# Kernel tuning notes

Measured on AMD Instinct MI355X. Metric: run time of the kernel, lower is better.

The kernel has to match this reference:

```python
import jax, jax.numpy as jnp
import numpy as np

DILATIONS = (1, 3, 6, 12)          # layer dilations, flattened from [[1,3],[6,12]]
BLOCKS = ((0, 1), (2, 3))           # block -> layer indices
H_SIZE = 32
STATE_SIZE = 128
OUT_SIZE = STATE_SIZE - H_SIZE      # 96
INPUT_SIZE = 64
OUTPUT_SIZE = 64
T, B = 512, 512


def _linear_params(k, fan_in, fan_out):
    bound = 1.0 / np.sqrt(fan_in)
    kw, kb = jax.random.split(k)
    W = jax.random.uniform(kw, (fan_out, fan_in), minval=-bound, maxval=bound, dtype=jnp.float32)
    b = jax.random.uniform(kb, (fan_out,), minval=-bound, maxval=bound, dtype=jnp.float32)
    return W, b


def setup_inputs() -> dict:
    key = jax.random.key(0)
    ks = jax.random.split(key, 8)
    x = jax.random.normal(ks[0], (T, B, INPUT_SIZE), dtype=jnp.float32)
    ins = [INPUT_SIZE, OUT_SIZE, OUT_SIZE, OUT_SIZE]  # first layer sees raw input
    out = {"x": x}
    for l in range(4):
        W, b = _linear_params(ks[1 + l], ins[l] + 2 * H_SIZE, 4 * STATE_SIZE)
        out[f"W{l}"] = W
        out[f"b{l}"] = b
    Wa, ba = _linear_params(ks[5], OUT_SIZE, OUTPUT_SIZE)
    out["Wa"] = Wa
    out["ba"] = ba
    return out


def _s2cell(W, b, inp, prev_h, second_h, prev_c, delayed_c, has_prev, has_del):
    # xh = cat(input, prev_h, delayed_h-or-prev_h) ; zeros when no prev state (handled by caller masks)
    xh = jnp.concatenate([inp, prev_h, second_h], axis=1)
    g = xh @ W.T + b                                     # [B, 4*state]
    g0, g1, g2, g3 = jnp.split(g, 4, axis=1)
    forget = jax.nn.sigmoid(g0 + 1.0)
    cand = jnp.tanh(g1)
    alpha = jax.nn.sigmoid(g2)
    out_gate = jax.nn.sigmoid(g3)
    weighted = jnp.where(has_del, alpha * prev_c + (1.0 - alpha) * delayed_c, prev_c)
    new_c = jnp.where(has_prev, forget * weighted + (1.0 - forget) * cand, cand)
    whole = out_gate * new_c
    return whole[:, :OUT_SIZE], whole[:, OUT_SIZE:], new_c


def reference(x, W0, b0, W1, b1, W2, b2, W3, b3, Wa, ba):
    Ws = [W0, W1, W2, W3]
    bs = [b0, b1, b2, b3]
    batch = x.shape[1]
    h0 = tuple(jnp.zeros((d, batch, H_SIZE), jnp.float32) for d in DILATIONS)
    c0 = tuple(jnp.zeros((d, batch, STATE_SIZE), jnp.float32) for d in DILATIONS)

    def step(carry, inp_t):
        t, h_bufs, c_bufs = carry
        h_bufs = list(h_bufs)
        c_bufs = list(c_bufs)
        has_prev = t >= 1
        prev_block = None
        out_t = None
        for iblock, layers in enumerate(BLOCKS):
            for j, l in enumerate(layers):
                cur_in = (inp_t if iblock == 0 else prev_block) if j == 0 else out_t
                d = DILATIONS[l]
                # ring buffer: slot (t-1)%d holds state at t-1, slot t%d still holds state at t-d
                prev_h = jnp.where(has_prev, h_bufs[l][(t - 1) % d], 0.0)
                prev_c = c_bufs[l][(t - 1) % d]
                has_del = t >= d
                del_h = jnp.where(has_del, h_bufs[l][t % d], prev_h)
                del_c = c_bufs[l][t % d]
                out_t, new_h, new_c = _s2cell(Ws[l], bs[l], cur_in, prev_h, del_h,
                                              prev_c, del_c, has_prev, has_del)
                h_bufs[l] = h_bufs[l].at[t % d].set(new_h)
                c_bufs[l] = c_bufs[l].at[t % d].set(new_c)
            prev_block = out_t if iblock == 0 else out_t + prev_block  # resnet shortcut
        y = prev_block @ Wa.T + ba
        return (t + 1, tuple(h_bufs), tuple(c_bufs)), y

    _, ys = jax.lax.scan(step, (jnp.int32(0), h0, c0), x)
    return ys  # [T, B, output_size]
```

## Files before the change

### kernel.cpp

```cpp
#include <hip/hip_runtime.h>

typedef unsigned int uint;
typedef unsigned short ushort;
typedef unsigned long long u64;
typedef __attribute__((ext_vector_type(8))) short bf16x8;
typedef __attribute__((ext_vector_type(4))) float f32x4;

#define T_STEPS 512
#define BATCH   512
#define NB      8
#define RD      16
#define XS      168
#define CSTR    12
#define OUTC    96
#define FSTR    32

__device__ __forceinline__ ushort f2bf(float f){
  uint u = __builtin_bit_cast(uint, f);
  u = (u + 0x7FFFu + ((u >> 16) & 1u)) >> 16;
  return (ushort)u;
}
__device__ __forceinline__ float bf2f(ushort h){
  uint u = ((uint)h) << 16; return __builtin_bit_cast(float, u);
}
__device__ __forceinline__ float sigm(float x){
  float e = __builtin_exp2f(-1.44269504f * x);
  return __builtin_amdgcn_rcpf(1.0f + e);
}
__device__ __forceinline__ float tanh_fast(float x){
  float e = __builtin_exp2f(-2.88539008f * x);
  return 2.0f * __builtin_amdgcn_rcpf(1.0f + e) - 1.0f;
}
__device__ __forceinline__ uint aload32(const uint* p){
  return __hip_atomic_load(p, __ATOMIC_RELAXED, __HIP_MEMORY_SCOPE_AGENT);
}
__device__ __forceinline__ void astore32(uint* p, uint v){
  __hip_atomic_store(p, v, __ATOMIC_RELAXED, __HIP_MEMORY_SCOPE_AGENT);
}
__device__ __forceinline__ u64 aload64(const u64* p){
  return __hip_atomic_load(p, __ATOMIC_RELAXED, __HIP_MEMORY_SCOPE_AGENT);
}
__device__ __forceinline__ void astore64(u64* p, u64 v){
  __hip_atomic_store(p, v, __ATOMIC_RELAXED, __HIP_MEMORY_SCOPE_AGENT);
}

__global__ __launch_bounds__(512, 1)
void rnn_pipeline(const float* __restrict__ x,
                  const float* __restrict__ W0, const float* __restrict__ b0,
                  const float* __restrict__ W1, const float* __restrict__ b1,
                  const float* __restrict__ W2, const float* __restrict__ b2,
                  const float* __restrict__ W3, const float* __restrict__ b3,
                  const float* __restrict__ Wa, const float* __restrict__ ba,
                  float* __restrict__ y_out,
                  uint* __restrict__ prod, uint* __restrict__ consA,
                  uint* __restrict__ consB,
                  u64* __restrict__ hop0, u64* __restrict__ hop1,
                  u64* __restrict__ hop2)
{
  const int tid  = threadIdx.x;
  const int wv   = tid >> 6;
  const int lane = tid & 63;
  const int l15  = lane & 15;
  const int hi   = lane >> 4;
  const int rep  = blockIdx.x & 63;
  const int stage= blockIdx.x >> 6;
  const int b0r  = rep * NB;

  const int dil = (stage==0)?1:(stage==1)?3:(stage==2)?6:12;
  const int KIN = (stage==0)?64:96;
  const int K   = KIN + 64;
  const float* Wl = (stage==0)?W0:(stage==1)?W1:(stage==2)?W2:W3;
  const float* bl = (stage==0)?b0:(stage==1)?b1:(stage==2)?b2:b3;

  __shared__ __align__(16) ushort xh_hi[16*XS], xh_lo[16*XS];
  __shared__ __align__(16) float  sh_c[12*128*CSTR];
  __shared__ __align__(16) ushort h_hi[12*NB*32], h_lo[12*NB*32];
  __shared__ __align__(16) ushort outp[2304];
  __shared__ __align__(16) ushort o1p[1536];
  __shared__ __align__(16) float  o3f[NB*OUTC];
  __shared__ __align__(16) float  yst[512];

  for (int i = tid; i < 16*XS; i += 512){ xh_hi[i] = 0; xh_lo[i] = 0; }
  for (int i = tid; i < 12*128*CSTR; i += 512) sh_c[i] = 0.0f;
  for (int i = tid; i < 12*NB*32; i += 512){ h_hi[i] = 0; h_lo[i] = 0; }
  for (int i = tid; i < 2304; i += 512) outp[i] = 0;
  for (int i = tid; i < 1536; i += 512) o1p[i] = 0;
  for (int i = tid; i < NB*OUTC; i += 512) o3f[i] = 0.0f;

  const int sidx = 16*wv + l15;

  bf16x8 whi[4][5], wlo[4][5];
  #pragma unroll
  for (int j = 0; j < 4; ++j){
    const int grow = 128*j + sidx;
    #pragma unroll
    for (int ks = 0; ks < 5; ++ks){
      bf16x8 vh, vl;
      const int cb = ks*32 + hi*8;
      if (cb < K){
        const float* p = Wl + (size_t)grow*K + cb;
        #pragma unroll
        for (int i = 0; i < 8; ++i){
          float w = p[i];
          ushort h = f2bf(w);
          vh[i] = (short)h;
          vl[i] = (short)f2bf(w - bf2f(h));
        }
      } else {
        #pragma unroll
        for (int i = 0; i < 8; ++i){ vh[i] = 0; vl[i] = 0; }
      }
      whi[j][ks] = vh; wlo[j][ks] = vl;
    }
  }
  float bias[4];
  #pragma unroll
  for (int j = 0; j < 4; ++j) bias[j] = bl[128*j + sidx];

  bf16x8 phi[3], plo[3];
  #pragma unroll
  for (int ks = 0; ks < 3; ++ks){
    bf16x8 z;
    #pragma unroll
    for (int i = 0; i < 8; ++i) z[i]=0;
    phi[ks]=z; plo[ks]=z;
  }
  float bav = 0.0f;
  if (stage == 3 && wv < 4){
    const int ocol = 16*wv + l15;
    #pragma unroll
    for (int ks = 0; ks < 3; ++ks){
      const float* p = Wa + (size_t)ocol*96 + ks*32 + hi*8;
      bf16x8 vh, vl;
      #pragma unroll
      for (int i = 0; i < 8; ++i){
        float w = p[i];
        ushort h = f2bf(w);
        vh[i] = (short)h;
        vl[i] = (short)f2bf(w - bf2f(h));
      }
      phi[ks] = vh; plo[ks] = vl;
    }
    bav = ba[ocol];
  }

  uint* up_prod  = (stage==1)? &prod[rep*FSTR] : (stage==2)? &prod[(64+rep)*FSTR] :
                   (stage==3)? &prod[(128+rep)*FSTR] : nullptr;
  uint* up_prod1 = (stage==3)? &prod[(64+rep)*FSTR] : nullptr;
  uint* my_prod  = (stage==0)? &prod[rep*FSTR] : (stage==1)? &prod[(64+rep)*FSTR] :
                   (stage==2)? &prod[(128+rep)*FSTR] : nullptr;
  uint* my_consA = (stage==1)? &consA[rep*FSTR] : (stage==2)? &consA[(64+rep)*FSTR] :
                   (stage==3)? &consA[(128+rep)*FSTR] : nullptr;
  uint* my_consB = (stage==3)? &consB[rep*FSTR] : nullptr;
  uint* dnA      = (stage==0)? &consA[rep*FSTR] : (stage==1)? &consA[(64+rep)*FSTR] :
                   (stage==2)? &consA[(128+rep)*FSTR] : nullptr;
  uint* dnB      = (stage==1)? &consB[rep*FSTR] : nullptr;
  const u64* hop_in  = (stage==1)? hop0 : (stage==2)? hop1 : nullptr;
  u64*       hop_out = (stage==0)? hop0 : (stage==1)? hop1 : (stage==2)? hop2 : nullptr;

  __syncthreads();

  u64 pfA = 0, pfB = 0; float xv = 0.0f;
  uint fvU = 0, fvU1 = 0, fvDA = 0, fvDB = 0;
  if (stage == 0){
    xv = x[(size_t)(b0r + (tid>>6))*64 + (tid&63)];
  } else if (stage < 3){
    do { fvU = aload32(up_prod); if (fvU < 3u) __builtin_amdgcn_s_sleep(2); } while (fvU < 3u);
    if (tid < 384) pfA = aload64(hop_in + (size_t)rep*384 + tid);
  } else {
    do { fvU  = aload32(up_prod);  if (fvU  < 3u) __builtin_amdgcn_s_sleep(2); } while (fvU  < 3u);
    do { fvU1 = aload32(up_prod1); if (fvU1 < 3u) __builtin_amdgcn_s_sleep(2); } while (fvU1 < 3u);
    const u64* s2 = hop2 + (size_t)rep*384;
    const u64* s1 = hop1 + (size_t)rep*384;
    pfA = (tid < 384) ? aload64(s2 + tid) : aload64(s1 + (tid - 384));
    if (tid < 256) pfB = aload64(s1 + 128 + tid);
  }

  int cur = 0, prv = dil - 1;
  for (int t = 0; t < T_STEPS; ++t){
    const int slot = t & (RD-1);

    if (stage < 3) asm volatile("s_waitcnt vmcnt(1)" ::: "memory");
    if (stage > 0){
      const bool bad = (fvU < (uint)(t+3)) || (stage==3 && fvU1 < (uint)(t+3));
      if (bad){
        if (lane == 0){
          while (aload32(up_prod) < (uint)(t+1)) __builtin_amdgcn_s_sleep(2);
          if (stage == 3)
            while (aload32(up_prod1) < (uint)(t+1)) __builtin_amdgcn_s_sleep(2);
        }
        if (stage < 3){
          if (tid < 384) pfA = aload64(hop_in + (size_t)(slot*64 + rep)*384 + tid);
        } else {
          const u64* s2 = hop2 + (size_t)(slot*64 + rep)*384;
          const u64* s1 = hop1 + (size_t)(slot*64 + rep)*384;
          pfA = (tid < 384) ? aload64(s2 + tid) : aload64(s1 + (tid - 384));
          if (tid < 256) pfB = aload64(s1 + 128 + tid);
        }
      }
    }
    if (stage == 0){
      const int r = tid >> 6, c = tid & 63;
      ushort hb = f2bf(xv);
      xh_hi[r*XS + c] = hb;
      xh_lo[r*XS + c] = f2bf(xv - bf2f(hb));
    } else {
      if (tid < 384){
        const int q = (tid < 192) ? tid : tid - 192;
        ushort* plane = (tid < 192) ? xh_hi : xh_lo;
        const int r = q / 24, c4 = (q % 24) * 4;
        *(u64*)(plane + r*XS + c4) = pfA;
      } else if (stage == 3){
        *(u64*)(o1p + 4*(tid - 384)) = pfA;
      }
      if (stage == 3 && tid < 256) *(u64*)(o1p + 4*(128 + tid)) = pfB;
    }
    {
      const int which = tid >> 8, rem = tid & 255, r = rem >> 5, c = rem & 31;
      const int srcslot = (which == 1 && t >= dil) ? cur : prv;
      xh_hi[r*XS + KIN + which*32 + c] = h_hi[srcslot*(NB*32) + r*32 + c];
      xh_lo[r*XS + KIN + which*32 + c] = h_lo[srcslot*(NB*32) + r*32 + c];
    }
    __syncthreads();
    if (tid == 0){
      if (stage > 0){
        astore32(my_consA, (uint)(t+1));
        if (stage == 3) astore32(my_consB, (uint)(t+1));
      }
      if (stage < 3 && t >= 1) astore32(my_prod, (uint)(t-1));
    }
    if (stage == 3 && t > 0){
      y_out[(size_t)((t-1)*BATCH + b0r + (tid>>6))*64 + (tid&63)] = yst[tid];
    }
    const bool pre = (t + 1 < T_STEPS);
    if (pre){
      const int ns = (t + 1) & (RD-1);
      if (stage == 0){
        xv = x[(size_t)((t+1)*BATCH + b0r + (tid>>6))*64 + (tid&63)];
      } else if (stage < 3){
        if (tid < 384) pfA = aload64(hop_in + (size_t)(ns*64 + rep)*384 + tid);
        fvU = aload32(up_prod);
      } else {
        const u64* s2 = hop2 + (size_t)(ns*64 + rep)*384;
        const u64* s1 = hop1 + (size_t)(ns*64 + rep)*384;
        pfA = (tid < 384) ? aload64(s2 + tid) : aload64(s1 + (tid - 384));
        if (tid < 256) pfB = aload64(s1 + 128 + tid);
        fvU  = aload32(up_prod);
        fvU1 = aload32(up_prod1);
      }
    }
    if (stage < 3) fvDA = aload32(dnA);
    if (stage == 1) fvDB = aload32(dnB);
    asm volatile("" ::: "memory");

    f32x4 acc[4];
    #pragma unroll
    for (int j = 0; j < 4; ++j) acc[j] = (f32x4){bias[j],bias[j],bias[j],bias[j]};
    const int abase = l15*XS + hi*8;
    #pragma unroll
    for (int ks = 0; ks < 5; ++ks){
      if (ks*32 < K){
        bf16x8 ahi = *(const bf16x8*)(xh_hi + abase + ks*32);
        bf16x8 alo = *(const bf16x8*)(xh_lo + abase + ks*32);
        #pragma unroll
        for (int j = 0; j < 4; ++j){
          acc[j] = __builtin_amdgcn_mfma_f32_16x16x32_bf16(ahi, whi[j][ks], acc[j], 0, 0, 0);
          acc[j] = __builtin_amdgcn_mfma_f32_16x16x32_bf16(alo, whi[j][ks], acc[j], 0, 0, 0);
          acc[j] = __builtin_amdgcn_mfma_f32_16x16x32_bf16(ahi, wlo[j][ks], acc[j], 0, 0, 0);
        }
      }
    }

    f32x4 pc = *(const f32x4*)(sh_c + prv*(128*CSTR) + sidx*CSTR + (hi&1)*4);
    f32x4 dc = *(const f32x4*)(sh_c + cur*(128*CSTR) + sidx*CSTR + (hi&1)*4);
    const bool has_prev = (t >= 1), has_del = (t >= dil);
    f32x4 ncv; float whv[4];
    #pragma unroll
    for (int k = 0; k < 4; ++k){
      float f  = sigm(acc[0][k] + 1.0f);
      float cd = tanh_fast(acc[1][k]);
      float al = sigm(acc[2][k]);
      float og = sigm(acc[3][k]);
      float wt = has_del ? (al*pc[k] + (1.0f - al)*dc[k]) : pc[k];
      float nc = has_prev ? (f*wt + (1.0f - f)*cd) : cd;
      ncv[k] = nc;
      whv[k] = og * nc;
    }
    if (hi < 2){
      *(f32x4*)(sh_c + cur*(128*CSTR) + sidx*CSTR + hi*4) = ncv;
      #pragma unroll
      for (int k = 0; k < 4; ++k){
        const int r = hi*4 + k;
        const float w = whv[k];
        if (sidx < OUTC){
          if (stage == 3){
            o3f[r*OUTC + sidx] = w;
          } else {
            ushort hb = f2bf(w);
            outp[r*OUTC + sidx]       = hb;
            outp[768 + r*OUTC + sidx] = f2bf(w - bf2f(hb));
          }
        } else {
          ushort hb = f2bf(w);
          h_hi[cur*(NB*32) + r*32 + (sidx - OUTC)] = hb;
          h_lo[cur*(NB*32) + r*32 + (sidx - OUTC)] = f2bf(w - bf2f(hb));
        }
      }
    }
    __syncthreads();

    if (stage < 3){
      if (t >= RD){
        const bool badc = (fvDA < (uint)(t-13)) || (stage==1 && fvDB < (uint)(t-13));
        if (badc){
          if (lane == 0){
            while (aload32(dnA) < (uint)(t-15)) __builtin_amdgcn_s_sleep(2);
            if (stage == 1)
              while (aload32(dnB) < (uint)(t-15)) __builtin_amdgcn_s_sleep(2);
          }
        }
      }
      if (lane < 48){
        const int g = wv*48 + lane;
        u64 v = *(const u64*)(outp + 4*g);
        astore64(hop_out + (size_t)(slot*64 + rep)*384 + g, v);
      }
    } else {
      for (int j = tid; j < 768; j += 512){
        float v = o3f[j] + bf2f(o1p[j]) + bf2f(o1p[768 + j]);
        ushort hb = f2bf(v);
        outp[j]       = hb;
        outp[768 + j] = f2bf(v - bf2f(hb));
      }
      __syncthreads();
      if (wv < 4){
        f32x4 acc1 = (f32x4){bav, bav, bav, bav};
        const int pbase = l15*96 + hi*8;
        #pragma unroll
        for (int ks = 0; ks < 3; ++ks){
          bf16x8 ahi = *(const bf16x8*)(outp + pbase + ks*32);
          bf16x8 alo = *(const bf16x8*)(outp + 768 + pbase + ks*32);
          acc1 = __builtin_amdgcn_mfma_f32_16x16x32_bf16(ahi, phi[ks], acc1, 0, 0, 0);
          acc1 = __builtin_amdgcn_mfma_f32_16x16x32_bf16(alo, phi[ks], acc1, 0, 0, 0);
          acc1 = __builtin_amdgcn_mfma_f32_16x16x32_bf16(ahi, plo[ks], acc1, 0, 0, 0);
        }
        if (hi < 2){
          const int ocol = 16*wv + l15;
          #pragma unroll
          for (int k = 0; k < 4; ++k){
            yst[(hi*4 + k)*64 + ocol] = acc1[k];
          }
        }
      }
    }
    prv = cur;
    cur = (cur + 1 == dil) ? 0 : cur + 1;
  }

  asm volatile("s_waitcnt vmcnt(0)" ::: "memory");
  __syncthreads();
  if (stage == 3){
    y_out[(size_t)((T_STEPS-1)*BATCH + b0r + (tid>>6))*64 + (tid&63)] = yst[tid];
  }
  if (stage < 3 && tid == 0) astore32(my_prod, (uint)(T_STEPS + 3));
}

extern "C" void kernel_launch(void* const* d_in, const int* in_sizes, int n_in,
                              void* d_out, int out_size, void* d_ws, size_t ws_size,
                              hipStream_t stream) {
  (void)in_sizes; (void)n_in; (void)out_size; (void)ws_size;
  const float* x  = (const float*)d_in[0];
  const float* W0 = (const float*)d_in[1];
  const float* b0 = (const float*)d_in[2];
  const float* W1 = (const float*)d_in[3];
  const float* b1 = (const float*)d_in[4];
  const float* W2 = (const float*)d_in[5];
  const float* b2 = (const float*)d_in[6];
  const float* W3 = (const float*)d_in[7];
  const float* b3 = (const float*)d_in[8];
  const float* Wa = (const float*)d_in[9];
  const float* ba = (const float*)d_in[10];
  float* out = (float*)d_out;

  uint* prod  = (uint*)d_ws;
  uint* consA = (uint*)((char*)d_ws + 24576);
  uint* consB = (uint*)((char*)d_ws + 49152);
  u64* hop0 = (u64*)((char*)d_ws + 65536);
  u64* hop1 = hop0 + (size_t)RD*64*384;
  u64* hop2 = hop1 + (size_t)RD*64*384;

  hipMemsetAsync(d_ws, 0, 65536, stream);
  hipLaunchKernelGGL(rnn_pipeline, dim3(256), dim3(512), 0, stream,
                     x, W0, b0, W1, b1, W2, b2, W3, b3, Wa, ba,
                     out, prod, consA, consB, hop0, hop1, hop2);
}
```

Baseline: 2.228 ms.

## Halve block size to 256 threads, doubling per-wave gate columns and MFMA work

Runs each pipeline stage block with 4 waves instead of 8, so each wave holds two 16-column groups of split-bf16 weights in registers and issues twice the MFMAs per step. All cooperative loops, hop-buffer loads and stores, and output writes are reindexed for 256 threads. The producer flag now publishes t instead of t-1, and the startup wait drops from 3 to 1. Prefetch waits tighten from vmcnt(1) to vmcnt(0). The goal is less per-step barrier and wave-coordination overhead in this latency-bound recurrence. The cost is doubled register pressure for weights and accumulators, longer serial per-wave compute, and a changed synchronisation protocol.

```diff
diff --git a/kernel.cpp b/kernel.cpp
--- a/kernel.cpp
+++ b/kernel.cpp
@@ -44,7 +44,7 @@
   __hip_atomic_store(p, v, __ATOMIC_RELAXED, __HIP_MEMORY_SCOPE_AGENT);
 }
 
-__global__ __launch_bounds__(512, 1)
+__global__ __launch_bounds__(256, 1)
 void rnn_pipeline(const float* __restrict__ x,
                   const float* __restrict__ W0, const float* __restrict__ b0,
                   const float* __restrict__ W1, const float* __restrict__ b1,
@@ -80,42 +80,48 @@
   __shared__ __align__(16) float  o3f[NB*OUTC];
   __shared__ __align__(16) float  yst[512];
 
-  for (int i = tid; i < 16*XS; i += 512){ xh_hi[i] = 0; xh_lo[i] = 0; }
-  for (int i = tid; i < 12*128*CSTR; i += 512) sh_c[i] = 0.0f;
-  for (int i = tid; i < 12*NB*32; i += 512){ h_hi[i] = 0; h_lo[i] = 0; }
-  for (int i = tid; i < 2304; i += 512) outp[i] = 0;
-  for (int i = tid; i < 1536; i += 512) o1p[i] = 0;
-  for (int i = tid; i < NB*OUTC; i += 512) o3f[i] = 0.0f;
-
-  const int sidx = 16*wv + l15;
-
-  bf16x8 whi[4][5], wlo[4][5];
+  for (int i = tid; i < 16*XS; i += 256){ xh_hi[i] = 0; xh_lo[i] = 0; }
+  for (int i = tid; i < 12*128*CSTR; i += 256) sh_c[i] = 0.0f;
+  for (int i = tid; i < 12*NB*32; i += 256){ h_hi[i] = 0; h_lo[i] = 0; }
+  for (int i = tid; i < 2304; i += 256) outp[i] = 0;
+  for (int i = tid; i < 1536; i += 256) o1p[i] = 0;
+  for (int i = tid; i < NB*OUTC; i += 256) o3f[i] = 0.0f;
+  yst[tid] = 0.0f; yst[tid + 256] = 0.0f;
+
+  const int sidx = 32*wv + l15;
+
+  bf16x8 whi[2][4][5], wlo[2][4][5];
   #pragma unroll
-  for (int j = 0; j < 4; ++j){
-    const int grow = 128*j + sidx;
-    #pragma unroll
-    for (int ks = 0; ks < 5; ++ks){
-      bf16x8 vh, vl;
-      const int cb = ks*32 + hi*8;
-      if (cb < K){
-        const float* p = Wl + (size_t)grow*K + cb;
-        #pragma unroll
-        for (int i = 0; i < 8; ++i){
-          float w = p[i];
-          ushort h = f2bf(w);
-          vh[i] = (short)h;
-          vl[i] = (short)f2bf(w - bf2f(h));
-        }
-      } else {
-        #pragma unroll
-        for (int i = 0; i < 8; ++i){ vh[i] = 0; vl[i] = 0; }
-      }
-      whi[j][ks] = vh; wlo[j][ks] = vl;
-    }
-  }
-  float bias[4];
+  for (int g = 0; g < 2; ++g){
+    #pragma unroll
+    for (int j = 0; j < 4; ++j){
+      const int grow = 128*j + sidx + 16*g;
+      #pragma unroll
+      for (int ks = 0; ks < 5; ++ks){
+        bf16x8 vh, vl;
+        const int cb = ks*32 + hi*8;
+        if (cb < K){
+          const float* p = Wl + (size_t)grow*K + cb;
+          #pragma unroll
+          for (int i = 0; i < 8; ++i){
+            float w = p[i];
+            ushort h = f2bf(w);
+            vh[i] = (short)h;
+            vl[i] = (short)f2bf(w - bf2f(h));
+          }
+        } else {
+          #pragma unroll
+          for (int i = 0; i < 8; ++i){ vh[i] = 0; vl[i] = 0; }
+        }
+        whi[g][j][ks] = vh; wlo[g][j][ks] = vl;
+      }
+    }
+  }
+  float bias[2][4];
   #pragma unroll
-  for (int j = 0; j < 4; ++j) bias[j] = bl[128*j + sidx];
+  for (int g = 0; g < 2; ++g)
+    #pragma unroll
+    for (int j = 0; j < 4; ++j) bias[g][j] = bl[128*j + sidx + 16*g];
 
   bf16x8 phi[3], plo[3];
   #pragma unroll
@@ -126,7 +132,7 @@
     phi[ks]=z; plo[ks]=z;
   }
   float bav = 0.0f;
-  if (stage == 3 && wv < 4){
+  if (stage == 3){
     const int ocol = 16*wv + l15;
     #pragma unroll
     for (int ks = 0; ks < 3; ++ks){
@@ -160,27 +166,30 @@
 
   __syncthreads();
 
-  u64 pfA = 0, pfB = 0; float xv = 0.0f;
+  u64 pfA = 0, pfB = 0, pfC = 0, pfD = 0;
+  float xv0 = 0.0f, xv1 = 0.0f;
   uint fvU = 0, fvU1 = 0, fvDA = 0, fvDB = 0;
   if (stage == 0){
-    xv = x[(size_t)(b0r + (tid>>6))*64 + (tid&63)];
+    xv0 = x[(size_t)(b0r + (tid>>6))*64 + (tid&63)];
+    xv1 = x[(size_t)(b0r + (tid>>6) + 4)*64 + (tid&63)];
   } else if (stage < 3){
-    do { fvU = aload32(up_prod); if (fvU < 3u) __builtin_amdgcn_s_sleep(2); } while (fvU < 3u);
-    if (tid < 384) pfA = aload64(hop_in + (size_t)rep*384 + tid);
+    do { fvU = aload32(up_prod); if (fvU < 1u) __builtin_amdgcn_s_sleep(2); } while (fvU < 1u);
+    pfA = aload64(hop_in + tid);
+    if (tid < 128) pfB = aload64(hop_in + 256 + tid);
   } else {
-    do { fvU  = aload32(up_prod);  if (fvU  < 3u) __builtin_amdgcn_s_sleep(2); } while (fvU  < 3u);
-    do { fvU1 = aload32(up_prod1); if (fvU1 < 3u) __builtin_amdgcn_s_sleep(2); } while (fvU1 < 3u);
-    const u64* s2 = hop2 + (size_t)rep*384;
-    const u64* s1 = hop1 + (size_t)rep*384;
-    pfA = (tid < 384) ? aload64(s2 + tid) : aload64(s1 + (tid - 384));
-    if (tid < 256) pfB = aload64(s1 + 128 + tid);
+    do { fvU  = aload32(up_prod);  if (fvU  < 1u) __builtin_amdgcn_s_sleep(2); } while (fvU  < 1u);
+    do { fvU1 = aload32(up_prod1); if (fvU1 < 1u) __builtin_amdgcn_s_sleep(2); } while (fvU1 < 1u);
+    pfA = aload64(hop2 + tid);
+    if (tid < 128) pfB = aload64(hop2 + 256 + tid);
+    pfC = aload64(hop1 + tid);
+    if (tid < 128) pfD = aload64(hop1 + 256 + tid);
   }
 
   int cur = 0, prv = dil - 1;
   for (int t = 0; t < T_STEPS; ++t){
     const int slot = t & (RD-1);
 
-    if (stage < 3) asm volatile("s_waitcnt vmcnt(1)" ::: "memory");
+    asm volatile("s_waitcnt vmcnt(0)" ::: "memory");
     if (stage > 0){
       const bool bad = (fvU < (uint)(t+3)) || (stage==3 && fvU1 < (uint)(t+3));
       if (bad){
@@ -190,36 +199,48 @@
             while (aload32(up_prod1) < (uint)(t+1)) __builtin_amdgcn_s_sleep(2);
         }
         if (stage < 3){
-          if (tid < 384) pfA = aload64(hop_in + (size_t)(slot*64 + rep)*384 + tid);
+          const u64* s = hop_in + (size_t)(slot*64 + rep)*384;
+          pfA = aload64(s + tid);
+          if (tid < 128) pfB = aload64(s + 256 + tid);
         } else {
           const u64* s2 = hop2 + (size_t)(slot*64 + rep)*384;
           const u64* s1 = hop1 + (size_t)(slot*64 + rep)*384;
-          pfA = (tid < 384) ? aload64(s2 + tid) : aload64(s1 + (tid - 384));
-          if (tid < 256) pfB = aload64(s1 + 128 + tid);
-        }
+          pfA = aload64(s2 + tid);
+          if (tid < 128) pfB = aload64(s2 + 256 + tid);
+          pfC = aload64(s1 + tid);
+          if (tid < 128) pfD = aload64(s1 + 256 + tid);
+        }
+        asm volatile("s_waitcnt vmcnt(0)" ::: "memory");
       }
     }
     if (stage == 0){
       const int r = tid >> 6, c = tid & 63;
-      ushort hb = f2bf(xv);
-      xh_hi[r*XS + c] = hb;
-      xh_lo[r*XS + c] = f2bf(xv - bf2f(hb));
+      ushort hb0 = f2bf(xv0);
+      xh_hi[r*XS + c] = hb0;       xh_lo[r*XS + c] = f2bf(xv0 - bf2f(hb0));
+      ushort hb1 = f2bf(xv1);
+      xh_hi[(r+4)*XS + c] = hb1;   xh_lo[(r+4)*XS + c] = f2bf(xv1 - bf2f(hb1));
     } else {
-      if (tid < 384){
-        const int q = (tid < 192) ? tid : tid - 192;
-        ushort* plane = (tid < 192) ? xh_hi : xh_lo;
-        const int r = q / 24, c4 = (q % 24) * 4;
-        *(u64*)(plane + r*XS + c4) = pfA;
-      } else if (stage == 3){
-        *(u64*)(o1p + 4*(tid - 384)) = pfA;
-      }
-      if (stage == 3 && tid < 256) *(u64*)(o1p + 4*(128 + tid)) = pfB;
+      {
+        const int q = tid, qq = (q < 192) ? q : q - 192;
+        ushort* plane = (q < 192) ? xh_hi : xh_lo;
+        *(u64*)(plane + (qq/24)*XS + (qq%24)*4) = pfA;
+      }
+      if (tid < 128){
+        const int q = tid + 256, qq = q - 192;
+        *(u64*)(xh_lo + (qq/24)*XS + (qq%24)*4) = pfB;
+      }
+      if (stage == 3){
+        *(u64*)(o1p + 4*tid) = pfC;
+        if (tid < 128) *(u64*)(o1p + 4*(tid + 256)) = pfD;
+      }
     }
     {
-      const int which = tid >> 8, rem = tid & 255, r = rem >> 5, c = rem & 31;
-      const int srcslot = (which == 1 && t >= dil) ? cur : prv;
-      xh_hi[r*XS + KIN + which*32 + c] = h_hi[srcslot*(NB*32) + r*32 + c];
-      xh_lo[r*XS + KIN + which*32 + c] = h_lo[srcslot*(NB*32) + r*32 + c];
+      const int r = tid >> 5, c = tid & 31;
+      xh_hi[r*XS + KIN + c] = h_hi[prv*(NB*32) + r*32 + c];
+      xh_lo[r*XS + KIN + c] = h_lo[prv*(NB*32) + r*32 + c];
+      const int ss = (t >= dil) ? cur : prv;
+      xh_hi[r*XS + KIN + 32 + c] = h_hi[ss*(NB*32) + r*32 + c];
+      xh_lo[r*XS + KIN + 32 + c] = h_lo[ss*(NB*32) + r*32 + c];
     }
     __syncthreads();
     if (tid == 0){
@@ -227,24 +248,30 @@
         astore32(my_consA, (uint)(t+1));
         if (stage == 3) astore32(my_consB, (uint)(t+1));
       }
-      if (stage < 3 && t >= 1) astore32(my_prod, (uint)(t-1));
+      if (stage < 3 && t >= 1) astore32(my_prod, (uint)t);
     }
     if (stage == 3 && t > 0){
       y_out[(size_t)((t-1)*BATCH + b0r + (tid>>6))*64 + (tid&63)] = yst[tid];
+      y_out[(size_t)((t-1)*BATCH + b0r + (tid>>6) + 4)*64 + (tid&63)] = yst[tid + 256];
     }
     const bool pre = (t + 1 < T_STEPS);
     if (pre){
       const int ns = (t + 1) & (RD-1);
       if (stage == 0){
-        xv = x[(size_t)((t+1)*BATCH + b0r + (tid>>6))*64 + (tid&63)];
+        xv0 = x[(size_t)((t+1)*BATCH + b0r + (tid>>6))*64 + (tid&63)];
+        xv1 = x[(size_t)((t+1)*BATCH + b0r + (tid>>6) + 4)*64 + (tid&63)];
       } else if (stage < 3){
-        if (tid < 384) pfA = aload64(hop_in + (size_t)(ns*64 + rep)*384 + tid);
+        const u64* s = hop_in + (size_t)(ns*64 + rep)*384;
+        pfA = aload64(s + tid);
+        if (tid < 128) pfB = aload64(s + 256 + tid);
         fvU = aload32(up_prod);
       } else {
         const u64* s2 = hop2 + (size_t)(ns*64 + rep)*384;
         const u64* s1 = hop1 + (size_t)(ns*64 + rep)*384;
-        pfA = (tid < 384) ? aload64(s2 + tid) : aload64(s1 + (tid - 384));
-        if (tid < 256) pfB = aload64(s1 + 128 + tid);
+        pfA = aload64(s2 + tid);
+        if (tid < 128) pfB = aload64(s2 + 256 + tid);
+        pfC = aload64(s1 + tid);
+        if (tid < 128) pfD = aload64(s1 + 256 + tid);
         fvU  = aload32(up_prod);
         fvU1 = aload32(up_prod1);
       }
@@ -253,9 +280,12 @@
     if (stage == 1) fvDB = aload32(dnB);
     asm volatile("" ::: "memory");
 
-    f32x4 acc[4];
-    #pragma unroll
-    for (int j = 0; j < 4; ++j) acc[j] = (f32x4){bias[j],bias[j],bias[j],bias[j]};
+    f32x4 acc[2][4];
+    #pragma unroll
+    for (int g = 0; g < 2; ++g)
+      #pragma unroll
+      for (int j = 0; j < 4; ++j)
+        acc[g][j] = (f32x4){bias[g][j],bias[g][j],bias[g][j],bias[g][j]};
     const int abase = l15*XS + hi*8;
     #pragma unroll
     for (int ks = 0; ks < 5; ++ks){
@@ -263,47 +293,54 @@
         bf16x8 ahi = *(const bf16x8*)(xh_hi + abase + ks*32);
         bf16x8 alo = *(const bf16x8*)(xh_lo + abase + ks*32);
         #pragma unroll
-        for (int j = 0; j < 4; ++j){
-          acc[j] = __builtin_amdgcn_mfma_f32_16x16x32_bf16(ahi, whi[j][ks], acc[j], 0, 0, 0);
-          acc[j] = __builtin_amdgcn_mfma_f32_16x16x32_bf16(alo, whi[j][ks], acc[j], 0, 0, 0);
-          acc[j] = __builtin_amdgcn_mfma_f32_16x16x32_bf16(ahi, wlo[j][ks], acc[j], 0, 0, 0);
-        }
-      }
-    }
-
-    f32x4 pc = *(const f32x4*)(sh_c + prv*(128*CSTR) + sidx*CSTR + (hi&1)*4);
-    f32x4 dc = *(const f32x4*)(sh_c + cur*(128*CSTR) + sidx*CSTR + (hi&1)*4);
+        for (int g = 0; g < 2; ++g){
+          #pragma unroll
+          for (int j = 0; j < 4; ++j){
+            acc[g][j] = __builtin_amdgcn_mfma_f32_16x16x32_bf16(ahi, whi[g][j][ks], acc[g][j], 0, 0, 0);
+            acc[g][j] = __builtin_amdgcn_mfma_f32_16x16x32_bf16(alo, whi[g][j][ks], acc[g][j], 0, 0, 0);
+            acc[g][j] = __builtin_amdgcn_mfma_f32_16x16x32_bf16(ahi, wlo[g][j][ks], acc[g][j], 0, 0, 0);
+          }
+        }
+      }
+    }
+
     const bool has_prev = (t >= 1), has_del = (t >= dil);
-    f32x4 ncv; float whv[4];
-    #pragma unroll
-    for (int k = 0; k < 4; ++k){
-      float f  = sigm(acc[0][k] + 1.0f);
-      float cd = tanh_fast(acc[1][k]);
-      float al = sigm(acc[2][k]);
-      float og = sigm(acc[3][k]);
-      float wt = has_del ? (al*pc[k] + (1.0f - al)*dc[k]) : pc[k];
-      float nc = has_prev ? (f*wt + (1.0f - f)*cd) : cd;
-      ncv[k] = nc;
-      whv[k] = og * nc;
-    }
-    if (hi < 2){
-      *(f32x4*)(sh_c + cur*(128*CSTR) + sidx*CSTR + hi*4) = ncv;
+    #pragma unroll
+    for (int g = 0; g < 2; ++g){
+      const int sg = sidx + 16*g;
+      f32x4 pc = *(const f32x4*)(sh_c + prv*(128*CSTR) + sg*CSTR + (hi&1)*4);
+      f32x4 dc = *(const f32x4*)(sh_c + cur*(128*CSTR) + sg*CSTR + (hi&1)*4);
+      f32x4 ncv; float whv[4];
       #pragma unroll
       for (int k = 0; k < 4; ++k){
-        const int r = hi*4 + k;
-        const float w = whv[k];
-        if (sidx < OUTC){
-          if (stage == 3){
-            o3f[r*OUTC + sidx] = w;
+        float f  = sigm(acc[g][0][k] + 1.0f);
+        float cd = tanh_fast(acc[g][1][k]);
+        float al = sigm(acc[g][2][k]);
+        float og = sigm(acc[g][3][k]);
+        float wt = has_del ? (al*pc[k] + (1.0f - al)*dc[k]) : pc[k];
+        float nc = has_prev ? (f*wt + (1.0f - f)*cd) : cd;
+        ncv[k] = nc;
+        whv[k] = og * nc;
+      }
+      if (hi < 2){
+        *(f32x4*)(sh_c + cur*(128*CSTR) + sg*CSTR + hi*4) = ncv;
+        #pragma unroll
+        for (int k = 0; k < 4; ++k){
+          const int r = hi*4 + k;
+          const float w = whv[k];
+          if (sg < OUTC){
+            if (stage == 3){
+              o3f[r*OUTC + sg] = w;
+            } else {
+              ushort hb = f2bf(w);
+              outp[r*OUTC + sg]       = hb;
+              outp[768 + r*OUTC + sg] = f2bf(w - bf2f(hb));
+            }
           } else {
             ushort hb = f2bf(w);
-            outp[r*OUTC + sidx]       = hb;
-            outp[768 + r*OUTC + sidx] = f2bf(w - bf2f(hb));
+            h_hi[cur*(NB*32) + r*32 + (sg - OUTC)] = hb;
+            h_lo[cur*(NB*32) + r*32 + (sg - OUTC)] = f2bf(w - bf2f(hb));
           }
-        } else {
-          ushort hb = f2bf(w);
-          h_hi[cur*(NB*32) + r*32 + (sidx - OUTC)] = hb;
-          h_lo[cur*(NB*32) + r*32 + (sidx - OUTC)] = f2bf(w - bf2f(hb));
         }
       }
     }
@@ -320,20 +357,18 @@
           }
         }
       }
-      if (lane < 48){
-        const int g = wv*48 + lane;
-        u64 v = *(const u64*)(outp + 4*g);
-        astore64(hop_out + (size_t)(slot*64 + rep)*384 + g, v);
-      }
+      u64* dst = hop_out + (size_t)(slot*64 + rep)*384;
+      astore64(dst + tid, *(const u64*)(outp + 4*tid));
+      if (tid < 128) astore64(dst + 256 + tid, *(const u64*)(outp + 4*(tid + 256)));
     } else {
-      for (int j = tid; j < 768; j += 512){
+      for (int j = tid; j < 768; j += 256){
         float v = o3f[j] + bf2f(o1p[j]) + bf2f(o1p[768 + j]);
         ushort hb = f2bf(v);
         outp[j]       = hb;
         outp[768 + j] = f2bf(v - bf2f(hb));
       }
       __syncthreads();
-      if (wv < 4){
+      {
         f32x4 acc1 = (f32x4){bav, bav, bav, bav};
         const int pbase = l15*96 + hi*8;
         #pragma unroll
@@ -361,6 +396,7 @@
   __syncthreads();
   if (stage == 3){
     y_out[(size_t)((T_STEPS-1)*BATCH + b0r + (tid>>6))*64 + (tid&63)] = yst[tid];
+    y_out[(size_t)((T_STEPS-1)*BATCH + b0r + (tid>>6) + 4)*64 + (tid&63)] = yst[tid + 256];
   }
   if (stage < 3 && tid == 0) astore32(my_prod, (uint)(T_STEPS + 3));
 }
@@ -390,7 +426,7 @@
   u64* hop2 = hop1 + (size_t)RD*64*384;
 
   hipMemsetAsync(d_ws, 0, 65536, stream);
-  hipLaunchKernelGGL(rnn_pipeline, dim3(256), dim3(512), 0, stream,
+  hipLaunchKernelGGL(rnn_pipeline, dim3(256), dim3(256), 0, stream,
                      x, W0, b0, W1, b1, W2, b2, W3, b3, Wa, ba,
                      out, prod, consA, consB, hop0, hop1, hop2);
 }
```

New measurement: 2.937 ms. +31.9%, slower.

## Deepen inter-stage prefetch to two steps with double-buffered registers

Applied to the files above, without the earlier changes.

Each pipeline stage now prefetches its upstream hop data (or its x input) two timesteps ahead, using alternating register buffers selected by step parity. The producer flag publication lags by two steps to match. The downstream-consumer wait moves from after the MFMA compute to before the prefetch issue. The aim is to hide global-memory latency between pipeline stages on the critical path, at the cost of more registers and a tighter flag protocol in which an off-by-one could cause stale reads. The removed explicit vmcnt wait and the added zero-init of yst also change the ordering assumptions.

```diff
diff --git a/kernel.cpp b/kernel.cpp
--- a/kernel.cpp
+++ b/kernel.cpp
@@ -86,6 +86,7 @@
   for (int i = tid; i < 2304; i += 512) outp[i] = 0;
   for (int i = tid; i < 1536; i += 512) o1p[i] = 0;
   for (int i = tid; i < NB*OUTC; i += 512) o3f[i] = 0.0f;
+  yst[tid] = 0.0f;
 
   const int sidx = 16*wv + l15;
 
@@ -158,62 +159,79 @@
   const u64* hop_in  = (stage==1)? hop0 : (stage==2)? hop1 : nullptr;
   u64*       hop_out = (stage==0)? hop0 : (stage==1)? hop1 : (stage==2)? hop2 : nullptr;
 
+  auto issueS12 = [&](u64& A, int sl){
+    if (tid < 384) A = aload64(hop_in + (size_t)(sl*64 + rep)*384 + tid);
+  };
+  auto issueS3 = [&](u64& A, u64& B, int sl){
+    const u64* s2 = hop2 + (size_t)(sl*64 + rep)*384;
+    const u64* s1 = hop1 + (size_t)(sl*64 + rep)*384;
+    A = (tid < 384) ? aload64(s2 + tid) : aload64(s1 + (tid - 384));
+    if (tid < 256) B = aload64(s1 + 128 + tid);
+  };
+  auto stageS12 = [&](u64 A){
+    if (tid < 384){
+      const int q = (tid < 192) ? tid : tid - 192;
+      ushort* pl = (tid < 192) ? xh_hi : xh_lo;
+      *(u64*)(pl + (q/24)*XS + (q%24)*4) = A;
+    }
+  };
+  auto stageS3 = [&](u64 A, u64 B){
+    if (tid < 384){
+      const int q = (tid < 192) ? tid : tid - 192;
+      ushort* pl = (tid < 192) ? xh_hi : xh_lo;
+      *(u64*)(pl + (q/24)*XS + (q%24)*4) = A;
+    } else {
+      *(u64*)(o1p + 4*(tid - 384)) = A;
+    }
+    if (tid < 256) *(u64*)(o1p + 4*(128 + tid)) = B;
+  };
+
   __syncthreads();
 
-  u64 pfA = 0, pfB = 0; float xv = 0.0f;
+  u64 pfA0 = 0, pfB0 = 0, pfA1 = 0, pfB1 = 0;
+  float xv0 = 0.0f, xv1 = 0.0f;
   uint fvU = 0, fvU1 = 0, fvDA = 0, fvDB = 0;
   if (stage == 0){
-    xv = x[(size_t)(b0r + (tid>>6))*64 + (tid&63)];
-  } else if (stage < 3){
-    do { fvU = aload32(up_prod); if (fvU < 3u) __builtin_amdgcn_s_sleep(2); } while (fvU < 3u);
-    if (tid < 384) pfA = aload64(hop_in + (size_t)rep*384 + tid);
+    xv0 = x[(size_t)(b0r + (tid>>6))*64 + (tid&63)];
+    xv1 = x[(size_t)(BATCH + b0r + (tid>>6))*64 + (tid&63)];
   } else {
-    do { fvU  = aload32(up_prod);  if (fvU  < 3u) __builtin_amdgcn_s_sleep(2); } while (fvU  < 3u);
-    do { fvU1 = aload32(up_prod1); if (fvU1 < 3u) __builtin_amdgcn_s_sleep(2); } while (fvU1 < 3u);
-    const u64* s2 = hop2 + (size_t)rep*384;
-    const u64* s1 = hop1 + (size_t)rep*384;
-    pfA = (tid < 384) ? aload64(s2 + tid) : aload64(s1 + (tid - 384));
-    if (tid < 256) pfB = aload64(s1 + 128 + tid);
+    do { fvU = aload32(up_prod); if (fvU < 4u) __builtin_amdgcn_s_sleep(2); } while (fvU < 4u);
+    if (stage == 3){
+      do { fvU1 = aload32(up_prod1); if (fvU1 < 4u) __builtin_amdgcn_s_sleep(2); } while (fvU1 < 4u);
+    }
+    if (stage < 3){ issueS12(pfA0, 0); issueS12(pfA1, 1); }
+    else          { issueS3(pfA0, pfB0, 0); issueS3(pfA1, pfB1, 1); }
   }
 
   int cur = 0, prv = dil - 1;
   for (int t = 0; t < T_STEPS; ++t){
     const int slot = t & (RD-1);
-
-    if (stage < 3) asm volatile("s_waitcnt vmcnt(1)" ::: "memory");
+    const bool even = ((t & 1) == 0);
+
     if (stage > 0){
-      const bool bad = (fvU < (uint)(t+3)) || (stage==3 && fvU1 < (uint)(t+3));
+      const bool bad = (fvU < (uint)(t+3)) || (stage == 3 && fvU1 < (uint)(t+3));
       if (bad){
         if (lane == 0){
           while (aload32(up_prod) < (uint)(t+1)) __builtin_amdgcn_s_sleep(2);
           if (stage == 3)
             while (aload32(up_prod1) < (uint)(t+1)) __builtin_amdgcn_s_sleep(2);
         }
-        if (stage < 3){
-          if (tid < 384) pfA = aload64(hop_in + (size_t)(slot*64 + rep)*384 + tid);
-        } else {
-          const u64* s2 = hop2 + (size_t)(slot*64 + rep)*384;
-          const u64* s1 = hop1 + (size_t)(slot*64 + rep)*384;
-          pfA = (tid < 384) ? aload64(s2 + tid) : aload64(s1 + (tid - 384));
-          if (tid < 256) pfB = aload64(s1 + 128 + tid);
-        }
+        if (stage < 3){ if (even) issueS12(pfA0, slot); else issueS12(pfA1, slot); }
+        else { if (even) issueS3(pfA0, pfB0, slot); else issueS3(pfA1, pfB1, slot); }
       }
     }
     if (stage == 0){
       const int r = tid >> 6, c = tid & 63;
-      ushort hb = f2bf(xv);
-      xh_hi[r*XS + c] = hb;
-      xh_lo[r*XS + c] = f2bf(xv - bf2f(hb));
+      if (even){
+        ushort hb = f2bf(xv0);
+        xh_hi[r*XS + c] = hb; xh_lo[r*XS + c] = f2bf(xv0 - bf2f(hb));
+      } else {
+        ushort hb = f2bf(xv1);
+        xh_hi[r*XS + c] = hb; xh_lo[r*XS + c] = f2bf(xv1 - bf2f(hb));
+      }
     } else {
-      if (tid < 384){
-        const int q = (tid < 192) ? tid : tid - 192;
-        ushort* plane = (tid < 192) ? xh_hi : xh_lo;
-        const int r = q / 24, c4 = (q % 24) * 4;
-        *(u64*)(plane + r*XS + c4) = pfA;
-      } else if (stage == 3){
-        *(u64*)(o1p + 4*(tid - 384)) = pfA;
-      }
-      if (stage == 3 && tid < 256) *(u64*)(o1p + 4*(128 + tid)) = pfB;
+      if (even){ if (stage < 3) stageS12(pfA0); else stageS3(pfA0, pfB0); }
+      else     { if (stage < 3) stageS12(pfA1); else stageS3(pfA1, pfB1); }
     }
     {
       const int which = tid >> 8, rem = tid & 255, r = rem >> 5, c = rem & 31;
@@ -227,28 +245,33 @@
         astore32(my_consA, (uint)(t+1));
         if (stage == 3) astore32(my_consB, (uint)(t+1));
       }
-      if (stage < 3 && t >= 1) astore32(my_prod, (uint)(t-1));
+      if (stage < 3 && t >= 2) astore32(my_prod, (uint)(t-2));
     }
     if (stage == 3 && t > 0){
       y_out[(size_t)((t-1)*BATCH + b0r + (tid>>6))*64 + (tid&63)] = yst[tid];
     }
-    const bool pre = (t + 1 < T_STEPS);
-    if (pre){
-      const int ns = (t + 1) & (RD-1);
+    if (stage < 3 && t >= RD){
+      const bool badc = (fvDA < (uint)(t-14)) || (stage == 1 && fvDB < (uint)(t-14));
+      if (badc){
+        if (lane == 0){
+          while (aload32(dnA) < (uint)(t-15)) __builtin_amdgcn_s_sleep(2);
+          if (stage == 1)
+            while (aload32(dnB) < (uint)(t-15)) __builtin_amdgcn_s_sleep(2);
+        }
+      }
+    }
+    if (t + 2 < T_STEPS){
+      const int ns = (t + 2) & (RD-1);
       if (stage == 0){
-        xv = x[(size_t)((t+1)*BATCH + b0r + (tid>>6))*64 + (tid&63)];
+        if (even) xv0 = x[(size_t)((t+2)*BATCH + b0r + (tid>>6))*64 + (tid&63)];
+        else      xv1 = x[(size_t)((t+2)*BATCH + b0r + (tid>>6))*64 + (tid&63)];
       } else if (stage < 3){
-        if (tid < 384) pfA = aload64(hop_in + (size_t)(ns*64 + rep)*384 + tid);
-        fvU = aload32(up_prod);
+        if (even) issueS12(pfA0, ns); else issueS12(pfA1, ns);
       } else {
-        const u64* s2 = hop2 + (size_t)(ns*64 + rep)*384;
-        const u64* s1 = hop1 + (size_t)(ns*64 + rep)*384;
-        pfA = (tid < 384) ? aload64(s2 + tid) : aload64(s1 + (tid - 384));
-        if (tid < 256) pfB = aload64(s1 + 128 + tid);
-        fvU  = aload32(up_prod);
-        fvU1 = aload32(up_prod1);
-      }
-    }
+        if (even) issueS3(pfA0, pfB0, ns); else issueS3(pfA1, pfB1, ns);
+      }
+    }
+    if (stage > 0){ fvU = aload32(up_prod); if (stage == 3) fvU1 = aload32(up_prod1); }
     if (stage < 3) fvDA = aload32(dnA);
     if (stage == 1) fvDB = aload32(dnB);
     asm volatile("" ::: "memory");
@@ -310,16 +333,6 @@
     __syncthreads();
 
     if (stage < 3){
-      if (t >= RD){
-        const bool badc = (fvDA < (uint)(t-13)) || (stage==1 && fvDB < (uint)(t-13));
-        if (badc){
-          if (lane == 0){
-            while (aload32(dnA) < (uint)(t-15)) __builtin_amdgcn_s_sleep(2);
-            if (stage == 1)
-              while (aload32(dnB) < (uint)(t-15)) __builtin_amdgcn_s_sleep(2);
-          }
-        }
-      }
       if (lane < 48){
         const int g = wv*48 + lane;
         u64 v = *(const u64*)(outp + 4*g);
```

After: 2.560 ms. 1.15x slower.
